# Performance work log

Measured on AMD Instinct MI355X. Metric: run time of the kernel, lower is better.

## Reference

```python
import jax, jax.numpy as jnp
import numpy as np

B = 64
H = W = 16
DIMS = [2048, 1024, 512, 256, 128, 1]


def setup_inputs() -> dict:
    key = jax.random.key(0)
    ks = jax.random.split(key, 11)
    inp = {"x": jax.random.normal(ks[0], (B, DIMS[0], H, W), dtype=jnp.float32)}
    for i in range(5):
        fan_in = DIMS[i]
        out = DIMS[i + 1]
        # per-sample weights [B, out, in, 1, 1], scaled ~1/sqrt(fan_in) to keep sigmoids unsaturated
        inp[f"fc{i+1}w"] = jax.random.normal(ks[1 + 2 * i], (B, out, fan_in, 1, 1), dtype=jnp.float32) / jnp.sqrt(jnp.float32(fan_in))
        inp[f"fc{i+1}b"] = jax.random.normal(ks[2 + 2 * i], (B, out), dtype=jnp.float32) * 0.1
    return inp


def _target_fc(h, w, b):
    # grouped 1x1 conv with groups=B == per-sample linear over channel dim
    # h: [B, in, H, W], w: [B, out, in, 1, 1], b: [B, out] -> [B, out, H, W]
    return jnp.einsum("boi,bihw->bohw", w[..., 0, 0], h) + b[:, :, None, None]


def reference(x, fc1w, fc1b, fc2w, fc2b, fc3w, fc3b, fc4w, fc4b, fc5w, fc5b):
    q = jax.nn.sigmoid(_target_fc(x, fc1w, fc1b))
    q = jax.nn.sigmoid(_target_fc(q, fc2w, fc2b))
    q = jax.nn.sigmoid(_target_fc(q, fc3w, fc3b))
    q = jax.nn.sigmoid(_target_fc(q, fc4w, fc4b))
    q = _target_fc(q, fc5w, fc5b)  # [B, 1, H, W]
    q = jnp.squeeze(q, axis=1)      # .squeeze() -> [B, H, W]
    return jax.nn.sigmoid(q)
```

## Files before the change

kernel.cpp:

```cpp
#include <hip/hip_runtime.h>
#include <hip/hip_bf16.h>
#include <hip/hip_fp16.h>


typedef __attribute__((ext_vector_type(4)))  float    f32x4;
typedef __attribute__((ext_vector_type(16))) float    f32x16;
typedef __attribute__((ext_vector_type(8)))  short    short8;
typedef __attribute__((ext_vector_type(4)))  short    short4v;
typedef __attribute__((ext_vector_type(8)))  _Float16 half8;

__device__ __forceinline__ unsigned short f2h_bits(float f) {
  return __builtin_bit_cast(unsigned short, (_Float16)f);
}
__device__ __forceinline__ float h2f(short h) {
  return (float)__builtin_bit_cast(_Float16, (unsigned short)h);
}

__global__ __launch_bounds__(256) void transpose_cvt(const float* __restrict__ X,
                                                     short* __restrict__ XT) {
  __shared__ float tile[32][33];
  const int b  = blockIdx.z;
  const int c0 = blockIdx.x * 32, s0 = blockIdx.y * 32;
  const int tl = threadIdx.x & 31, tw = threadIdx.x >> 5;
  const float* xp = X + ((size_t)b * 2048 + c0) * 256 + s0;
#pragma unroll
  for (int i = 0; i < 4; ++i) {
    const int c = tw * 4 + i;
    tile[c][tl] = xp[(size_t)c * 256 + tl];
  }
  __syncthreads();
  short* op = XT + ((size_t)(b * 256 + s0)) * 2048 + c0;
#pragma unroll
  for (int i = 0; i < 4; ++i) {
    const int s = tw * 4 + i;
    op[(size_t)s * 2048 + tl] = (short)f2h_bits(tile[tl][s]);
  }
}

struct WFrag { f32x4 v[8]; };

template <int M, int K, int WAVES, int NSPLIT>
__global__ __launch_bounds__(WAVES * 64, 2) void gemm_layer(
    const float* __restrict__ W, const float* __restrict__ bias,
    const short* __restrict__ Xin, short* __restrict__ Out) {
  constexpr int BK    = 64;
  constexpr int KH    = BK / 16;
  constexpr int NT    = K / BK;
  constexpr int NCG   = 8 / NSPLIT;
  constexpr int TILES = NCG * KH;
  constexpr int BM    = WAVES * 32;
  constexpr int MT    = M / BM;
  constexpr int TPW   = TILES / WAVES;
  constexpr int NS    = 256 / NSPLIT;
  constexpr int EPIW  = 40;

  __shared__ __align__(16) short lds[2][TILES * 512];
  __shared__ __align__(16) short epi[WAVES][32][EPIW];

  const int tid = threadIdx.x;
  const int w = tid >> 6, l = tid & 63;
  const int lr = l & 31;
  const int lh = l >> 5;

  const int per_b = MT * NSPLIT;
  const int b   = blockIdx.x / per_b;
  const int rem = blockIdx.x % per_b;
  const int mt  = rem / NSPLIT;
  const int ns  = rem % NSPLIT;
  const int m0  = mt * BM + w * 32;

  const float* Wb = W + ((size_t)b * M + m0) * K;
  const short* Xb = Xin + (size_t)b * 256 * K + (size_t)ns * NS * K;

  f32x16 acc[NCG] = {};

  auto stage = [&](int buf, int t) {
    const int k0 = t * BK;
#pragma unroll
    for (int i = 0; i < TPW; ++i) {
      const int T  = w * TPW + i;
      const int s  = (T / KH) * 32 + lr;
      const int kk = (T % KH) * 16 + (lh << 3);
      const short* src = Xb + (size_t)s * K + k0 + kk;
      __builtin_amdgcn_global_load_lds(
          (const __attribute__((address_space(1))) void*)src,
          (__attribute__((address_space(3))) void*)&lds[buf][T * 512],
          16, 0, 0);
    }
  };

  const float* wrow = Wb + (size_t)lr * K + (lh << 3);
  auto load_wfrag = [&](int t) {
    WFrag f;
#pragma unroll
    for (int h = 0; h < KH; ++h) {
      const float* wp = wrow + t * BK + h * 16;
      f.v[2 * h]     = *(const f32x4*)wp;
      f.v[2 * h + 1] = *(const f32x4*)(wp + 4);
    }
    return f;
  };

  WFrag wc = load_wfrag(0);
  stage(0, 0);
  __syncthreads();

  int cur = 0;
  for (int t = 0; t < NT; ++t) {
    WFrag wn;
    if (t + 1 < NT) wn = load_wfrag(t + 1);
    if (t + 1 < NT) stage(cur ^ 1, t + 1);
#pragma unroll
    for (int h = 0; h < KH; ++h) {
      half8 af;
#pragma unroll
      for (int j = 0; j < 4; ++j) {
        af[j]     = (_Float16)wc.v[2 * h][j];
        af[j + 4] = (_Float16)wc.v[2 * h + 1][j];
      }
#pragma unroll
      for (int cg = 0; cg < NCG; ++cg) {
        const short8 braw = *(const short8*)&lds[cur][(cg * KH + h) * 512 + l * 8];
        acc[cg] = __builtin_amdgcn_mfma_f32_32x32x16_f16(af, __builtin_bit_cast(half8, braw),
                                                         acc[cg], 0, 0, 0);
      }
    }
    __syncthreads();
    if (t + 1 < NT) wc = wn;
    cur ^= 1;
  }

  float brow[16];
#pragma unroll
  for (int r = 0; r < 16; ++r) {
    const int row = (r & 3) + 8 * (r >> 2) + (lh << 2);
    brow[r] = bias[(size_t)b * M + m0 + row];
  }
  const int s_loc = l >> 1, hi = l & 1;
#pragma unroll
  for (int cg = 0; cg < NCG; ++cg) {
#pragma unroll
    for (int rg = 0; rg < 4; ++rg) {
      short4v pk;
#pragma unroll
      for (int j = 0; j < 4; ++j) {
        const int r = rg * 4 + j;
        float v = acc[cg][r] + brow[r];
        v = 1.0f / (1.0f + __expf(-v));
        pk[j] = (short)f2h_bits(v);
      }
      *(short4v*)&epi[w][lr][rg * 8 + (lh << 2)] = pk;
    }
    const short8 r0 = *(const short8*)&epi[w][s_loc][hi * 16];
    const short8 r1 = *(const short8*)&epi[w][s_loc][hi * 16 + 8];
    short* op = Out + ((size_t)b * 256 + ns * NS + cg * 32 + s_loc) * M + m0 + hi * 16;
    *(short8*)op       = r0;
    *(short8*)(op + 8) = r1;
  }
}

__global__ __launch_bounds__(256) void fc5_sig(const float* __restrict__ W5,
                                               const float* __restrict__ B5,
                                               const short* __restrict__ H4,
                                               float* __restrict__ out) {
  const int tid = blockIdx.x * 256 + threadIdx.x;
  const int oi = tid >> 3;
  const int r  = tid & 7;
  const int b  = oi >> 8;
  const short* hp = H4 + ((size_t)oi << 7) + r * 16;
  const float* wp = W5 + b * 128 + r * 16;
  const short8 hh0 = *(const short8*)hp;
  const short8 hh1 = *(const short8*)(hp + 8);
  const f32x4 w0 = *(const f32x4*)wp;
  const f32x4 w1 = *(const f32x4*)(wp + 4);
  const f32x4 w2 = *(const f32x4*)(wp + 8);
  const f32x4 w3 = *(const f32x4*)(wp + 12);
  float a = 0.f;
#pragma unroll
  for (int j = 0; j < 4; ++j) a += h2f(hh0[j]) * w0[j];
#pragma unroll
  for (int j = 0; j < 4; ++j) a += h2f(hh0[j + 4]) * w1[j];
#pragma unroll
  for (int j = 0; j < 4; ++j) a += h2f(hh1[j]) * w2[j];
#pragma unroll
  for (int j = 0; j < 4; ++j) a += h2f(hh1[j + 4]) * w3[j];
  a += __shfl_xor(a, 1);
  a += __shfl_xor(a, 2);
  a += __shfl_xor(a, 4);
  if (r == 0) out[oi] = 1.0f / (1.0f + __expf(-(a + B5[b])));
}

extern "C" void kernel_launch(void* const* d_in, const int* in_sizes, int n_in,
                              void* d_out, int out_size, void* d_ws, size_t ws_size,
                              hipStream_t stream) {
  const float* x  = (const float*)d_in[0];
  const float* w1 = (const float*)d_in[1];  const float* b1 = (const float*)d_in[2];
  const float* w2 = (const float*)d_in[3];  const float* b2 = (const float*)d_in[4];
  const float* w3 = (const float*)d_in[5];  const float* b3 = (const float*)d_in[6];
  const float* w4 = (const float*)d_in[7];  const float* b4 = (const float*)d_in[8];
  const float* w5 = (const float*)d_in[9];  const float* b5 = (const float*)d_in[10];

  char* ws = (char*)d_ws;
  short* bufA = (short*)ws;
  short* bufB = (short*)(ws + (size_t)67108864);
  float* out  = (float*)d_out;

  transpose_cvt<<<dim3(64, 8, 64), 256, 0, stream>>>(x, bufA);
  gemm_layer<1024, 2048, 4, 1><<<512, 256, 0, stream>>>(w1, b1, bufA, bufB);
  gemm_layer<512, 1024, 2, 1><<<512, 128, 0, stream>>>(w2, b2, bufB, bufA);
  gemm_layer<256, 512, 2, 2><<<512, 128, 0, stream>>>(w3, b3, bufA, bufB);
  gemm_layer<128, 256, 1, 2><<<512, 64, 0, stream>>>(w4, b4, bufB, bufA);
  fc5_sig<<<512, 256, 0, stream>>>(w5, b5, bufA, out);
}
```

Before: 345.0 us.

## Deepen GEMM pipeline with manual vmcnt waits and pre-converted fp16 weights

Restructures the GEMM main loop so LDS staging runs two K-tiles ahead instead of one. Each iteration's __syncthreads is replaced by an explicit s_waitcnt vmcnt(8) plus a raw s_barrier, so the weight-fragment loads for the next tile can stay in flight across the barrier. The fp32-to-fp16 weight conversion moves out of the MFMA loop into a separate step after the barrier, keeping the inner loop to LDS reads and MFMAs. The hand-tuned wait counts and sched_barriers depend on the exact order in which loads are issued, so any change to TPW or the load order could break correctness silently.

```diff
diff --git a/kernel.cpp b/kernel.cpp
--- a/kernel.cpp
+++ b/kernel.cpp
@@ -101,33 +101,57 @@
     return f;
   };
 
-  WFrag wc = load_wfrag(0);
+  WFrag wn;
+  half8 wcH[KH];
+  auto cvtW = [&]() {
+#pragma unroll
+    for (int h = 0; h < KH; ++h) {
+#pragma unroll
+      for (int j = 0; j < 4; ++j) {
+        wcH[h][j]     = (_Float16)wn.v[2 * h][j];
+        wcH[h][j + 4] = (_Float16)wn.v[2 * h + 1][j];
+      }
+    }
+  };
+
   stage(0, 0);
-  __syncthreads();
-
-  int cur = 0;
+  asm volatile("" ::: "memory");
+  wn = load_wfrag(0);
+  asm volatile("" ::: "memory");
+  stage(1, 1);
+  asm volatile("" ::: "memory");
+  cvtW();
+  wn = load_wfrag(1);
+  asm volatile("" ::: "memory");
+  asm volatile("s_barrier" ::: "memory");
+  __builtin_amdgcn_sched_barrier(0);
+
   for (int t = 0; t < NT; ++t) {
-    WFrag wn;
-    if (t + 1 < NT) wn = load_wfrag(t + 1);
-    if (t + 1 < NT) stage(cur ^ 1, t + 1);
+    const int cur = t & 1;
 #pragma unroll
     for (int h = 0; h < KH; ++h) {
-      half8 af;
-#pragma unroll
-      for (int j = 0; j < 4; ++j) {
-        af[j]     = (_Float16)wc.v[2 * h][j];
-        af[j + 4] = (_Float16)wc.v[2 * h + 1][j];
-      }
 #pragma unroll
       for (int cg = 0; cg < NCG; ++cg) {
         const short8 braw = *(const short8*)&lds[cur][(cg * KH + h) * 512 + l * 8];
-        acc[cg] = __builtin_amdgcn_mfma_f32_32x32x16_f16(af, __builtin_bit_cast(half8, braw),
+        acc[cg] = __builtin_amdgcn_mfma_f32_32x32x16_f16(wcH[h], __builtin_bit_cast(half8, braw),
                                                          acc[cg], 0, 0, 0);
       }
     }
-    __syncthreads();
-    if (t + 1 < NT) wc = wn;
-    cur ^= 1;
+    if (t + 1 < NT) {
+      asm volatile("s_waitcnt vmcnt(8)" ::: "memory");
+      __builtin_amdgcn_sched_barrier(0);
+      asm volatile("s_barrier" ::: "memory");
+      __builtin_amdgcn_sched_barrier(0);
+      if (t + 2 < NT) {
+        stage(cur, t + 2);
+        asm volatile("" ::: "memory");
+      }
+      cvtW();
+      if (t + 2 < NT) {
+        wn = load_wfrag(t + 2);
+        asm volatile("" ::: "memory");
+      }
+    }
   }
 
   float brow[16];
```

Result: no change. 340.9 us (-1.2%).
